# Optimization experiments

Measured on AMD Instinct MI355X. Metric: run time of the kernel, lower is better.

## Reference

```python
import jax, jax.numpy as jnp
import numpy as np

N, E, D, H = 50000, 500000, 128, 128


def setup_inputs() -> dict:
    key = jax.random.key(0)
    ks = jax.random.split(key, 20)
    s = 0.05
    inp = {
        "node_states": jax.random.normal(ks[0], (N, D), jnp.float32),
        "edge_features": jax.random.normal(ks[1], (E, D), jnp.float32),
        "from_idx": jax.random.randint(ks[2], (E,), 0, N, dtype=jnp.int32),
        "to_idx": jax.random.randint(ks[3], (E,), 0, N, dtype=jnp.int32),
        "graph_idx": jax.random.randint(ks[4], (N,), 0, 16, dtype=jnp.int32),
        # message MLP: Linear(3D,H)-ReLU-Linear(H,H)-ReLU-Linear(H,D)
        "mW1": jax.random.normal(ks[5], (3 * D, H), jnp.float32) * s,
        "mb1": jnp.zeros((H,), jnp.float32),
        "mW2": jax.random.normal(ks[6], (H, H), jnp.float32) * s,
        "mb2": jnp.zeros((H,), jnp.float32),
        "mW3": jax.random.normal(ks[7], (H, D), jnp.float32) * s,
        "mb3": jnp.zeros((D,), jnp.float32),
    }
    # three GRU cells; W: input->gates [D,3D], U: hidden->gates [D,3D]; gate order r,z,n (torch)
    for i, g in enumerate(["g0", "g1", "g2"]):
        inp[g + "W"] = jax.random.normal(ks[8 + 2 * i], (D, 3 * D), jnp.float32) * s
        inp[g + "U"] = jax.random.normal(ks[9 + 2 * i], (D, 3 * D), jnp.float32) * s
        inp[g + "b"] = jnp.zeros((3 * D,), jnp.float32)
        inp[g + "c"] = jnp.zeros((3 * D,), jnp.float32)
    return inp


def _mlp(x, W1, b1, W2, b2, W3, b3):
    h = jax.nn.relu(x @ W1 + b1)
    h = jax.nn.relu(h @ W2 + b2)
    return h @ W3 + b3


def _gru(x, h, W, U, b, c):
    gi = x @ W + b  # [N,3D]
    gh = h @ U + c
    ir, iz, inn = jnp.split(gi, 3, axis=1)
    hr, hz, hn = jnp.split(gh, 3, axis=1)
    r = jax.nn.sigmoid(ir + hr)
    z = jax.nn.sigmoid(iz + hz)
    n = jnp.tanh(inn + r * hn)
    return (1.0 - z) * n + z * h


def reference(node_states, edge_features, from_idx, to_idx, graph_idx,
              mW1, mb1, mW2, mb2, mW3, mb3,
              g0W, g0U, g0b, g0c, g1W, g1U, g1b, g1c, g2W, g2U, g2b, g2c):
    n_nodes = node_states.shape[0]

    def prop_once(fi, ti):
        edge_in = jnp.concatenate(
            [node_states[fi], node_states[ti], edge_features], axis=1)  # [E,3D]
        edge_states = _mlp(edge_in, mW1, mb1, mW2, mb2, mW3, mb3)  # [E,D]
        return jax.ops.segment_sum(edge_states, ti, num_segments=n_nodes)

    # forward uses self.message_net for BOTH directions (reverse net unused)
    agg = prop_once(from_idx, to_idx) + prop_once(to_idx, from_idx)  # [N,D]

    h1 = _gru(node_states, agg, g0W, g0U, g0b, g0c)
    h2 = _gru(agg, h1, g1W, g1U, g1b, g1c)
    h3 = _gru(h1, h2, g2W, g2U, g2b, g2c)
    return h3
```

## Files before the change

### kernel.cpp

```cpp
#include <hip/hip_runtime.h>

typedef unsigned short u16;
typedef __attribute__((ext_vector_type(8))) short bf16x8;
typedef __attribute__((ext_vector_type(4))) float f32x4;

__device__ inline u16 f2bf(float f) {
  unsigned int u = __float_as_uint(f);
  u += 0x7fffu + ((u >> 16) & 1u);
  return (u16)(u >> 16);
}
__device__ inline float bf2f(u16 v) {
  return __uint_as_float((unsigned)v << 16);
}

__device__ inline uint4 pack8(float4 a, float4 b) {
  uint4 r;
  r.x = (unsigned)f2bf(a.x) | ((unsigned)f2bf(a.y) << 16);
  r.y = (unsigned)f2bf(a.z) | ((unsigned)f2bf(a.w) << 16);
  r.z = (unsigned)f2bf(b.x) | ((unsigned)f2bf(b.y) << 16);
  r.w = (unsigned)f2bf(b.z) | ((unsigned)f2bf(b.w) << 16);
  return r;
}

struct TransDesc {
  const float* src[9];
  u16* dst[9];
  int R[9];
  int C[9];
  int pre[10];
};

__global__ void transpose_all_kernel(TransDesc td) {
  int t = blockIdx.x * 256 + threadIdx.x;
  if (t >= td.pre[9]) return;
  int seg = 0;
  while (t >= td.pre[seg + 1]) ++seg;
  int local = t - td.pre[seg];
  int C = td.C[seg], R = td.R[seg];
  int r = local / C, c = local - r * C;
  td.dst[seg][(size_t)c * R + r] = f2bf(td.src[seg][local]);
}

__global__ void count_kernel(const int* __restrict__ fi,
                             const int* __restrict__ ti,
                             int* __restrict__ cnt, int E) {
  int e = blockIdx.x * 256 + threadIdx.x;
  if (e < E) {
    atomicAdd(&cnt[ti[e]], 1);
    atomicAdd(&cnt[fi[e]], 1);
  }
}

__global__ void scan1_kernel(const int* __restrict__ cnt,
                             int* __restrict__ partial, int N, int chunk) {
  __shared__ int sdata[256];
  int b = blockIdx.x, t = threadIdx.x;
  int base = b * chunk;
  int sum = 0;
  for (int i = t; i < chunk; i += 256) {
    int idx = base + i;
    if (idx < N) sum += cnt[idx];
  }
  sdata[t] = sum;
  __syncthreads();
  for (int s2 = 128; s2 > 0; s2 >>= 1) {
    if (t < s2) sdata[t] += sdata[t + s2];
    __syncthreads();
  }
  if (t == 0) partial[b] = sdata[0];
}

__global__ void scan2_kernel(int* __restrict__ partial) {
  __shared__ int s[256];
  int t = threadIdx.x;
  int own = partial[t];
  s[t] = own;
  __syncthreads();
  for (int d2 = 1; d2 < 256; d2 <<= 1) {
    int v = (t >= d2) ? s[t - d2] : 0;
    __syncthreads();
    s[t] += v;
    __syncthreads();
  }
  partial[t] = s[t] - own;
}

__global__ void scan3_kernel(const int* __restrict__ cnt,
                             const int* __restrict__ partialEx,
                             int* __restrict__ cursor, int N, int chunk) {
  __shared__ int s[256];
  int b = blockIdx.x, t = threadIdx.x;
  int base = b * chunk;
  int own = (t < chunk && base + t < N) ? cnt[base + t] : 0;
  s[t] = own;
  __syncthreads();
  for (int d2 = 1; d2 < 256; d2 <<= 1) {
    int v = (t >= d2) ? s[t - d2] : 0;
    __syncthreads();
    s[t] += v;
    __syncthreads();
  }
  int ex = s[t] - own + partialEx[b];
  if (t < chunk && base + t < N) cursor[base + t] = ex;
}

__global__ void slot_kernel(const int* __restrict__ fi,
                            const int* __restrict__ ti,
                            int* __restrict__ cursor, int* __restrict__ s_nbr,
                            int* __restrict__ s_eid, int* __restrict__ s_dest,
                            int E) {
  int e = blockIdx.x * 256 + threadIdx.x;
  if (e < E) {
    int f = fi[e], t2 = ti[e];
    int p0 = atomicAdd(&cursor[t2], 1);
    s_nbr[p0] = f;
    s_eid[p0] = e;
    s_dest[p0] = t2;
    int p1 = atomicAdd(&cursor[f], 1);
    s_nbr[p1] = t2;
    s_eid[p1] = e;
    s_dest[p1] = f;
  }
}

__device__ inline void stage_w_rw(u16* sW, const u16* __restrict__ src,
                                  int roww, int colofs, int tid) {
  int n = tid >> 1, half = tid & 1;
  const u16* s = src + (size_t)n * roww + colofs + half * 64;
#pragma unroll
  for (int q = 0; q < 8; ++q) {
    uint4 v = *(const uint4*)(s + q * 8);
    int byte = n * 256 + ((half * 128 + q * 16) ^ ((n & 7) << 4));
    *(uint4*)((char*)sW + byte) = v;
  }
}

__device__ inline void mfma_pass(const u16* A, const u16* W, f32x4 acc[8],
                                 int w, int lane) {
  const int cA = lane & 15;
  const int ko = (lane >> 4) * 8;
  const int arow = 16 * w + cA;
#pragma unroll
  for (int kk = 0; kk < 4; ++kk) {
    int ka = (kk * 32 + ko) * 2;
    int sx = ka ^ ((cA & 7) << 4);
    bf16x8 a = *(const bf16x8*)((const char*)A + arow * 256 + sx);
#pragma unroll
    for (int nt = 0; nt < 8; ++nt) {
      bf16x8 bb = *(const bf16x8*)((const char*)W + (nt * 16 + cA) * 256 + sx);
      acc[nt] = __builtin_amdgcn_mfma_f32_16x16x32_bf16(a, bb, acc[nt], 0, 0, 0);
    }
  }
}

__device__ inline void write_h_lds(u16* sH, const f32x4 acc[8], int w,
                                   int lane) {
#pragma unroll
  for (int nt = 0; nt < 8; ++nt) {
    int col = nt * 16 + (lane & 15);
#pragma unroll
    for (int i = 0; i < 4; ++i) {
      int rr = 16 * w + ((lane >> 4) * 4) + i;
      *(u16*)((char*)sH + rr * 256 + ((col * 2) ^ ((rr & 7) << 4))) =
          f2bf(acc[nt][i]);
    }
  }
}

__global__ __launch_bounds__(256) void node_partial_kernel(
    const float* __restrict__ ns, const u16* __restrict__ Wt1,
    u16* __restrict__ Pa, u16* __restrict__ Pb, int N) {
  __shared__ u16 sA[64 * 128];
  __shared__ u16 sW[128 * 128];
  const int tid = threadIdx.x;
  const int lane = tid & 63;
  const int w = tid >> 6;
  const int r0 = blockIdx.x * 64;
  {
    int row = tid >> 2, seg = tid & 3;
    int rr = r0 + row;
    if (rr >= N) rr = N - 1;
    const float4* sx = (const float4*)(ns + (size_t)rr * 128 + seg * 32);
#pragma unroll
    for (int q = 0; q < 4; ++q) {
      int byte = row * 256 + ((seg * 64 + q * 16) ^ ((row & 7) << 4));
      *(uint4*)((char*)sA + byte) = pack8(sx[q * 2], sx[q * 2 + 1]);
    }
  }
  stage_w_rw(sW, Wt1, 384, 0, tid);
  __syncthreads();
  f32x4 accA[8] = {};
  mfma_pass(sA, sW, accA, w, lane);
  __syncthreads();
  stage_w_rw(sW, Wt1, 384, 128, tid);
  __syncthreads();
  f32x4 accB[8] = {};
  mfma_pass(sA, sW, accB, w, lane);
#pragma unroll
  for (int nt = 0; nt < 8; ++nt) {
    int col = nt * 16 + (lane & 15);
#pragma unroll
    for (int i = 0; i < 4; ++i) {
      int rr = 16 * w + ((lane >> 4) * 4) + i;
      int row = r0 + rr;
      if (row < N) {
        Pa[(size_t)row * 128 + col] = f2bf(accA[nt][i]);
        Pb[(size_t)row * 128 + col] = f2bf(accB[nt][i]);
      }
    }
  }
}

__global__ __launch_bounds__(256) void efgemm_kernel(
    const float* __restrict__ ef, const u16* __restrict__ Wt1,
    const float* __restrict__ b1, u16* __restrict__ EFm, int E) {
  __shared__ u16 sA[64 * 128];
  __shared__ u16 sW[128 * 128];
  const int tid = threadIdx.x;
  const int lane = tid & 63;
  const int w = tid >> 6;
  const int r0 = blockIdx.x * 64;
  {
    int row = tid >> 2, seg = tid & 3;
    int rr = r0 + row;
    if (rr >= E) rr = E - 1;
    const float4* sx = (const float4*)(ef + (size_t)rr * 128 + seg * 32);
#pragma unroll
    for (int q = 0; q < 4; ++q) {
      int byte = row * 256 + ((seg * 64 + q * 16) ^ ((row & 7) << 4));
      *(uint4*)((char*)sA + byte) = pack8(sx[q * 2], sx[q * 2 + 1]);
    }
  }
  stage_w_rw(sW, Wt1, 384, 256, tid);
  __syncthreads();
  f32x4 acc[8] = {};
  mfma_pass(sA, sW, acc, w, lane);
  __syncthreads();
#pragma unroll
  for (int nt = 0; nt < 8; ++nt) {
    int col = nt * 16 + (lane & 15);
    float bv = b1[col];
#pragma unroll
    for (int i = 0; i < 4; ++i) {
      int rr = 16 * w + ((lane >> 4) * 4) + i;
      *(u16*)((char*)sA + rr * 256 + ((col * 2) ^ ((rr & 7) << 4))) =
          f2bf(acc[nt][i] + bv);
    }
  }
  __syncthreads();
#pragma unroll
  for (int it = 0; it < 4; ++it) {
    int task = tid + (it << 8);
    int row = task >> 4, c8 = task & 15;
    int gr = r0 + row;
    if (gr < E) {
      uint4 v = *(const uint4*)((const char*)sA + row * 256 +
                                ((c8 << 4) ^ ((row & 7) << 4)));
      *(uint4*)(EFm + (size_t)gr * 128 + (c8 << 3)) = v;
    }
  }
}

__global__ __launch_bounds__(512, 2) void edge_csr_kernel(
    const u16* __restrict__ EFm, const int* __restrict__ s_nbr,
    const int* __restrict__ s_eid, const int* __restrict__ s_dest,
    const u16* __restrict__ Wt2, const u16* __restrict__ Wt3,
    const u16* __restrict__ Pa, const u16* __restrict__ Pb,
    const float* __restrict__ b2, const float* __restrict__ b3,
    float* __restrict__ aggf, int nslots, int ntiles) {
  __shared__ u16 sH[128 * 128];
  __shared__ int sNbr[128];
  __shared__ int sEid[128];
  __shared__ int sDest[128];
  const int tid = threadIdx.x;
  const int lane = tid & 63;
  const int wv = tid >> 6;
  const int mw = wv >> 1;
  const int nw = wv & 1;
  const int l15 = lane & 15;
  const int lhi = lane >> 4;

  float b2f[4], b3f[4];
#pragma unroll
  for (int nt = 0; nt < 4; ++nt) {
    int col = (nw << 6) + (nt << 4) + l15;
    b2f[nt] = b2[col];
    b3f[nt] = b3[col];
  }
  bf16x8 w2f[4][4], w3f[4][4];
#pragma unroll
  for (int nt = 0; nt < 4; ++nt) {
    int c = (nw << 6) + (nt << 4) + l15;
#pragma unroll
    for (int kk = 0; kk < 4; ++kk) {
      w2f[nt][kk] = *(const bf16x8*)(Wt2 + (size_t)c * 128 + (kk << 5) + (lhi << 3));
      w3f[nt][kk] = *(const bf16x8*)(Wt3 + (size_t)c * 128 + (kk << 5) + (lhi << 3));
    }
  }
  __syncthreads();

  for (int t = blockIdx.x; t < ntiles; t += gridDim.x) {
    const int r0 = t << 7;
    if (tid < 128) {
      int r = r0 + tid;
      int rc = r < nslots ? r : nslots - 1;
      sNbr[tid] = s_nbr[rc];
      sEid[tid] = s_eid[rc];
      sDest[tid] = (r < nslots) ? s_dest[rc] : -1;
    }
    __syncthreads();
#pragma unroll
    for (int it = 0; it < 4; ++it) {
      int row = (tid >> 4) + (it << 5);
      int c8 = tid & 15;
      int nbr = sNbr[row], eid = sEid[row];
      int dst = sDest[row];
      if (dst < 0) dst = 0;
      uint4 efv = *(const uint4*)(EFm + (size_t)eid * 128 + (c8 << 3));
      uint4 pav = *(const uint4*)(Pa + (size_t)nbr * 128 + (c8 << 3));
      uint4 pbv = *(const uint4*)(Pb + (size_t)dst * 128 + (c8 << 3));
      const u16* pe = (const u16*)&efv;
      const u16* pa = (const u16*)&pav;
      const u16* pb = (const u16*)&pbv;
      unsigned o[4];
#pragma unroll
      for (int j = 0; j < 4; ++j) {
        float v0 = fmaxf(bf2f(pe[2 * j]) + bf2f(pa[2 * j]) + bf2f(pb[2 * j]), 0.f);
        float v1 = fmaxf(bf2f(pe[2 * j + 1]) + bf2f(pa[2 * j + 1]) + bf2f(pb[2 * j + 1]), 0.f);
        o[j] = (unsigned)f2bf(v0) | ((unsigned)f2bf(v1) << 16);
      }
      *(uint4*)((char*)sH + row * 256 + ((c8 << 4) ^ ((row & 7) << 4))) = *(uint4*)o;
    }
    __syncthreads();
    bf16x8 hA[2][4];
#pragma unroll
    for (int m = 0; m < 2; ++m) {
      int ra = (mw << 5) + (m << 4) + l15;
#pragma unroll
      for (int kk = 0; kk < 4; ++kk) {
        int sx = ((kk << 6) + (lhi << 4)) ^ ((ra & 7) << 4);
        hA[m][kk] = *(const bf16x8*)((const char*)sH + ra * 256 + sx);
      }
    }
    f32x4 acc2[2][4] = {};
#pragma unroll
    for (int kk = 0; kk < 4; ++kk)
#pragma unroll
      for (int nt = 0; nt < 4; ++nt)
#pragma unroll
        for (int m = 0; m < 2; ++m)
          acc2[m][nt] = __builtin_amdgcn_mfma_f32_16x16x32_bf16(
              hA[m][kk], w2f[nt][kk], acc2[m][nt], 0, 0, 0);
    __syncthreads();
#pragma unroll
    for (int m = 0; m < 2; ++m) {
#pragma unroll
      for (int i = 0; i < 4; ++i) {
        int rl = (mw << 5) + (m << 4) + (lhi << 2) + i;
#pragma unroll
        for (int nt = 0; nt < 4; ++nt) {
          int col = (nw << 6) + (nt << 4) + l15;
          float v = fmaxf(acc2[m][nt][i] + b2f[nt], 0.f);
          *(u16*)((char*)sH + rl * 256 + ((col * 2) ^ ((rl & 7) << 4))) = f2bf(v);
        }
      }
    }
    __syncthreads();
#pragma unroll
    for (int m = 0; m < 2; ++m) {
      int ra = (mw << 5) + (m << 4) + l15;
#pragma unroll
      for (int kk = 0; kk < 4; ++kk) {
        int sx = ((kk << 6) + (lhi << 4)) ^ ((ra & 7) << 4);
        hA[m][kk] = *(const bf16x8*)((const char*)sH + ra * 256 + sx);
      }
    }
    f32x4 acc3[2][4] = {};
#pragma unroll
    for (int kk = 0; kk < 4; ++kk)
#pragma unroll
      for (int nt = 0; nt < 4; ++nt)
#pragma unroll
        for (int m = 0; m < 2; ++m)
          acc3[m][nt] = __builtin_amdgcn_mfma_f32_16x16x32_bf16(
              hA[m][kk], w3f[nt][kk], acc3[m][nt], 0, 0, 0);
    __syncthreads();
#pragma unroll
    for (int m = 0; m < 2; ++m) {
#pragma unroll
      for (int i = 0; i < 4; ++i) {
        int rl = (mw << 5) + (m << 4) + (lhi << 2) + i;
#pragma unroll
        for (int nt = 0; nt < 4; ++nt) {
          int col = (nw << 6) + (nt << 4) + l15;
          *(u16*)((char*)sH + rl * 256 + ((col * 2) ^ ((rl & 7) << 4))) =
              f2bf(acc3[m][nt][i] + b3f[nt]);
        }
      }
    }
    __syncthreads();
    {
      int c = tid & 127, q = tid >> 7;
      float s = 0.f;
      int prev = -1;
      int rbeg = q << 5;
#pragma unroll 4
      for (int rr = rbeg; rr < rbeg + 32; ++rr) {
        int d = sDest[rr];
        if (d != prev) {
          if (prev >= 0) unsafeAtomicAdd(&aggf[(size_t)prev * 128 + c], s);
          prev = d;
          s = 0.f;
        }
        if (d >= 0)
          s += bf2f(*(const u16*)((const char*)sH + rr * 256 +
                                  ((c * 2) ^ ((rr & 7) << 4))));
      }
      if (prev >= 0) unsafeAtomicAdd(&aggf[(size_t)prev * 128 + c], s);
    }
    __syncthreads();
  }
}

__global__ __launch_bounds__(256, 2) void gru3_kernel(
    const float* __restrict__ ns, const float* __restrict__ aggf,
    const u16* __restrict__ g0W, const u16* __restrict__ g0U,
    const u16* __restrict__ g1W, const u16* __restrict__ g1U,
    const u16* __restrict__ g2W, const u16* __restrict__ g2U,
    const float* __restrict__ b0, const float* __restrict__ c0,
    const float* __restrict__ b1, const float* __restrict__ c1,
    const float* __restrict__ b2, const float* __restrict__ c2,
    float* __restrict__ out, int N) {
  __shared__ u16 sX[64 * 128];
  __shared__ u16 sG[64 * 128];
  __shared__ u16 sW[128 * 128];
  const int tid = threadIdx.x;
  const int lane = tid & 63;
  const int w = tid >> 6;
  const int r0 = blockIdx.x * 64;
  {
    int row = tid >> 2, seg = tid & 3;
    int rr = r0 + row;
    if (rr >= N) rr = N - 1;
    const float4* sx = (const float4*)(ns + (size_t)rr * 128 + seg * 32);
    const float4* sh = (const float4*)(aggf + (size_t)rr * 128 + seg * 32);
#pragma unroll
    for (int q = 0; q < 4; ++q) {
      int byte = row * 256 + ((seg * 64 + q * 16) ^ ((row & 7) << 4));
      *(uint4*)((char*)sX + byte) = pack8(sx[q * 2], sx[q * 2 + 1]);
      *(uint4*)((char*)sG + byte) = pack8(sh[q * 2], sh[q * 2 + 1]);
    }
  }

  float hpf[8][4];

#define GPASS(SRC, ABUF, ACC)                       \
  __syncthreads();                                  \
  stage_w_rw(sW, (SRC), 128, 0, tid);               \
  __syncthreads();                                  \
  mfma_pass((ABUF), sW, (ACC), w, lane);

  {
    f32x4 ar[8] = {}, az[8] = {}, ai[8] = {}, ah[8] = {};
    GPASS(g0W + 0 * 16384, sX, ar)
    GPASS(g0U + 0 * 16384, sG, ar)
    GPASS(g0W + 1 * 16384, sX, az)
    GPASS(g0U + 1 * 16384, sG, az)
    GPASS(g0W + 2 * 16384, sX, ai)
    GPASS(g0U + 2 * 16384, sG, ah)
    f32x4 h1[8];
#pragma unroll
    for (int nt = 0; nt < 8; ++nt) {
      int col = nt * 16 + (lane & 15);
      float brc = b0[col] + c0[col];
      float bzc = b0[128 + col] + c0[128 + col];
      float bi = b0[256 + col];
      float bc2 = c0[256 + col];
#pragma unroll
      for (int i = 0; i < 4; ++i) {
        int rloc = 16 * w + ((lane >> 4) * 4) + i;
        int row = r0 + rloc;
        int rowc = row < N ? row : N - 1;
        float hf = aggf[(size_t)rowc * 128 + col];
        float rg = 1.f / (1.f + __expf(-(ar[nt][i] + brc)));
        float zg = 1.f / (1.f + __expf(-(az[nt][i] + bzc)));
        float pre = ai[nt][i] + bi + rg * (ah[nt][i] + bc2);
        float ng = 2.f / (1.f + __expf(-2.f * pre)) - 1.f;
        float hv = (1.f - zg) * ng + zg * hf;
        h1[nt][i] = hv;
        hpf[nt][i] = hv;
      }
    }
    write_h_lds(sX, h1, w, lane);
  }
  {
    f32x4 ar[8] = {}, az[8] = {}, ai[8] = {}, ah[8] = {};
    GPASS(g1W + 0 * 16384, sG, ar)
    GPASS(g1U + 0 * 16384, sX, ar)
    GPASS(g1W + 1 * 16384, sG, az)
    GPASS(g1U + 1 * 16384, sX, az)
    GPASS(g1W + 2 * 16384, sG, ai)
    GPASS(g1U + 2 * 16384, sX, ah)
    f32x4 h2[8];
#pragma unroll
    for (int nt = 0; nt < 8; ++nt) {
      int col = nt * 16 + (lane & 15);
      float brc = b1[col] + c1[col];
      float bzc = b1[128 + col] + c1[128 + col];
      float bi = b1[256 + col];
      float bc2 = c1[256 + col];
#pragma unroll
      for (int i = 0; i < 4; ++i) {
        float rg = 1.f / (1.f + __expf(-(ar[nt][i] + brc)));
        float zg = 1.f / (1.f + __expf(-(az[nt][i] + bzc)));
        float pre = ai[nt][i] + bi + rg * (ah[nt][i] + bc2);
        float ng = 2.f / (1.f + __expf(-2.f * pre)) - 1.f;
        float hv = (1.f - zg) * ng + zg * hpf[nt][i];
        h2[nt][i] = hv;
        hpf[nt][i] = hv;
      }
    }
    write_h_lds(sG, h2, w, lane);
  }
  {
    f32x4 ar[8] = {}, az[8] = {}, ai[8] = {}, ah[8] = {};
    GPASS(g2W + 0 * 16384, sX, ar)
    GPASS(g2U + 0 * 16384, sG, ar)
    GPASS(g2W + 1 * 16384, sX, az)
    GPASS(g2U + 1 * 16384, sG, az)
    GPASS(g2W + 2 * 16384, sX, ai)
    GPASS(g2U + 2 * 16384, sG, ah)
#pragma unroll
    for (int nt = 0; nt < 8; ++nt) {
      int col = nt * 16 + (lane & 15);
      float brc = b2[col] + c2[col];
      float bzc = b2[128 + col] + c2[128 + col];
      float bi = b2[256 + col];
      float bc2 = c2[256 + col];
#pragma unroll
      for (int i = 0; i < 4; ++i) {
        int rloc = 16 * w + ((lane >> 4) * 4) + i;
        int row = r0 + rloc;
        if (row < N) {
          float rg = 1.f / (1.f + __expf(-(ar[nt][i] + brc)));
          float zg = 1.f / (1.f + __expf(-(az[nt][i] + bzc)));
          float pre = ai[nt][i] + bi + rg * (ah[nt][i] + bc2);
          float ng = 2.f / (1.f + __expf(-2.f * pre)) - 1.f;
          out[(size_t)row * 128 + col] = (1.f - zg) * ng + zg * hpf[nt][i];
        }
      }
    }
  }
#undef GPASS
}

extern "C" void kernel_launch(void* const* d_in, const int* in_sizes, int n_in,
                              void* d_out, int out_size, void* d_ws,
                              size_t ws_size, hipStream_t stream) {
  const float* ns = (const float*)d_in[0];
  const float* ef = (const float*)d_in[1];
  const int* from_idx = (const int*)d_in[2];
  const int* to_idx = (const int*)d_in[3];
  const float* mW1 = (const float*)d_in[5];
  const float* mb1 = (const float*)d_in[6];
  const float* mW2 = (const float*)d_in[7];
  const float* mb2 = (const float*)d_in[8];
  const float* mW3 = (const float*)d_in[9];
  const float* mb3 = (const float*)d_in[10];
  const float* gW[3] = {(const float*)d_in[11], (const float*)d_in[15], (const float*)d_in[19]};
  const float* gU[3] = {(const float*)d_in[12], (const float*)d_in[16], (const float*)d_in[20]};
  const float* gb[3] = {(const float*)d_in[13], (const float*)d_in[17], (const float*)d_in[21]};
  const float* gc[3] = {(const float*)d_in[14], (const float*)d_in[18], (const float*)d_in[22]};

  const int N = in_sizes[0] / 128;
  const int E = in_sizes[1] / 128;
  const int nslots = 2 * E;

  char* base = (char*)d_ws;
  size_t cur = 0;
  auto alloc = [&](size_t bytes) {
    size_t p = cur;
    cur = (cur + bytes + 255) & ~(size_t)255;
    return (void*)(base + p);
  };
  float* aggf = (float*)alloc((size_t)N * 128 * 4);
  u16* Pa = (u16*)alloc((size_t)N * 128 * 2);
  u16* Pb = (u16*)alloc((size_t)N * 128 * 2);
  u16* Wt1 = (u16*)alloc(384 * 128 * 2);
  u16* Wt2 = (u16*)alloc(128 * 128 * 2);
  u16* Wt3 = (u16*)alloc(128 * 128 * 2);
  u16 *gWt[3], *gUt[3];
  for (int i = 0; i < 3; ++i) {
    gWt[i] = (u16*)alloc(384 * 128 * 2);
    gUt[i] = (u16*)alloc(384 * 128 * 2);
  }
  int* cnt = (int*)alloc((size_t)N * 4);
  int* cursor = (int*)alloc((size_t)N * 4);
  int* partial = (int*)alloc(256 * 4);
  int* s_nbr = (int*)alloc((size_t)nslots * 4);
  int* s_eid = (int*)alloc((size_t)nslots * 4);
  int* s_dest = (int*)alloc((size_t)nslots * 4);
  u16* EFm = (u16*)alloc((size_t)E * 128 * 2);
  (void)ws_size;

  {
    TransDesc td;
    const float* srcs[9] = {mW1, mW2, mW3, gW[0], gU[0], gW[1], gU[1], gW[2], gU[2]};
    u16* dsts[9] = {Wt1, Wt2, Wt3, gWt[0], gUt[0], gWt[1], gUt[1], gWt[2], gUt[2]};
    int Rs[9] = {384, 128, 128, 128, 128, 128, 128, 128, 128};
    int Cs[9] = {128, 128, 128, 384, 384, 384, 384, 384, 384};
    int acc = 0;
    for (int i = 0; i < 9; ++i) {
      td.src[i] = srcs[i];
      td.dst[i] = dsts[i];
      td.R[i] = Rs[i];
      td.C[i] = Cs[i];
      td.pre[i] = acc;
      acc += Rs[i] * Cs[i];
    }
    td.pre[9] = acc;
    transpose_all_kernel<<<(acc + 255) / 256, 256, 0, stream>>>(td);
  }

  node_partial_kernel<<<(N + 63) / 64, 256, 0, stream>>>(ns, Wt1, Pa, Pb, N);

  hipMemsetAsync(cnt, 0, (size_t)N * 4, stream);
  count_kernel<<<(E + 255) / 256, 256, 0, stream>>>(from_idx, to_idx, cnt, E);
  int chunk = (N + 255) / 256;
  scan1_kernel<<<256, 256, 0, stream>>>(cnt, partial, N, chunk);
  scan2_kernel<<<1, 256, 0, stream>>>(partial);
  scan3_kernel<<<256, 256, 0, stream>>>(cnt, partial, cursor, N, chunk);
  slot_kernel<<<(E + 255) / 256, 256, 0, stream>>>(from_idx, to_idx, cursor,
                                                   s_nbr, s_eid, s_dest, E);

  efgemm_kernel<<<(E + 63) / 64, 256, 0, stream>>>(ef, Wt1, mb1, EFm, E);

  hipMemsetAsync(aggf, 0, (size_t)N * 128 * 4, stream);
  int ntiles = (nslots + 127) / 128;
  int egrid = ntiles < 512 ? ntiles : 512;
  edge_csr_kernel<<<egrid, 512, 0, stream>>>(EFm, s_nbr, s_eid, s_dest, Wt2,
                                             Wt3, Pa, Pb, mb2, mb3, aggf,
                                             nslots, ntiles);

  int gblocks = (N + 63) / 64;
  gru3_kernel<<<gblocks, 256, 0, stream>>>(
      ns, aggf, gWt[0], gUt[0], gWt[1], gUt[1], gWt[2], gUt[2], gb[0], gc[0],
      gb[1], gc[1], gb[2], gc[2], (float*)d_out, N);
}
```

Baseline: 648.9 us.

## Prefetch next edge tile's gathers into LDS asynchronously and widen efgemm tiles

The edge MLP kernel now loads the next tile's slot metadata into registers. It then issues that tile's EFm, Pa and Pb row gathers straight into three new LDS buffers with global_load_lds, so the gather latency overlaps with the current tile's two MFMA layers and the atomic scatter. The extra 96 KB of LDS leaves room for only one 512-thread block per CU, so the persistent grid is cut to 256 blocks. Separately, the edge-feature GEMM now processes 128 rows per 512-thread block, with a matching weight-staging helper. Risks are lower occupancy, and the reliance on correct vmcnt waiting before the prefetched LDS data is read.

Measured after the change: 640.2 us. No clear change (-1.3%).

```diff
diff --git a/kernel.cpp b/kernel.cpp
--- a/kernel.cpp
+++ b/kernel.cpp
@@ -20,6 +20,12 @@
   r.z = (unsigned)f2bf(b.x) | ((unsigned)f2bf(b.y) << 16);
   r.w = (unsigned)f2bf(b.z) | ((unsigned)f2bf(b.w) << 16);
   return r;
+}
+
+__device__ inline void gload_lds16(const void* g, void* l) {
+  __builtin_amdgcn_global_load_lds(
+      (const __attribute__((address_space(1))) unsigned int*)g,
+      (__attribute__((address_space(3))) unsigned int*)l, 16, 0, 0);
 }
 
 struct TransDesc {
@@ -135,6 +141,18 @@
   }
 }
 
+__device__ inline void stage_w_512(u16* sW, const u16* __restrict__ src,
+                                   int roww, int colofs, int tid) {
+  int n = tid >> 2, quarter = tid & 3;
+  const u16* s = src + (size_t)n * roww + colofs + quarter * 32;
+#pragma unroll
+  for (int q = 0; q < 4; ++q) {
+    uint4 v = *(const uint4*)(s + q * 8);
+    int byte = n * 256 + ((quarter * 64 + q * 16) ^ ((n & 7) << 4));
+    *(uint4*)((char*)sW + byte) = v;
+  }
+}
+
 __device__ inline void mfma_pass(const u16* A, const u16* W, f32x4 acc[8],
                                  int w, int lane) {
   const int cA = lane & 15;
@@ -211,15 +229,15 @@
   }
 }
 
-__global__ __launch_bounds__(256) void efgemm_kernel(
+__global__ __launch_bounds__(512) void efgemm_kernel(
     const float* __restrict__ ef, const u16* __restrict__ Wt1,
     const float* __restrict__ b1, u16* __restrict__ EFm, int E) {
-  __shared__ u16 sA[64 * 128];
+  __shared__ u16 sA[128 * 128];
   __shared__ u16 sW[128 * 128];
   const int tid = threadIdx.x;
   const int lane = tid & 63;
   const int w = tid >> 6;
-  const int r0 = blockIdx.x * 64;
+  const int r0 = blockIdx.x * 128;
   {
     int row = tid >> 2, seg = tid & 3;
     int rr = r0 + row;
@@ -231,7 +249,7 @@
       *(uint4*)((char*)sA + byte) = pack8(sx[q * 2], sx[q * 2 + 1]);
     }
   }
-  stage_w_rw(sW, Wt1, 384, 256, tid);
+  stage_w_512(sW, Wt1, 384, 256, tid);
   __syncthreads();
   f32x4 acc[8] = {};
   mfma_pass(sA, sW, acc, w, lane);
@@ -250,7 +268,7 @@
   __syncthreads();
 #pragma unroll
   for (int it = 0; it < 4; ++it) {
-    int task = tid + (it << 8);
+    int task = tid + (it << 9);
     int row = task >> 4, c8 = task & 15;
     int gr = r0 + row;
     if (gr < E) {
@@ -269,8 +287,9 @@
     const float* __restrict__ b2, const float* __restrict__ b3,
     float* __restrict__ aggf, int nslots, int ntiles) {
   __shared__ u16 sH[128 * 128];
-  __shared__ int sNbr[128];
-  __shared__ int sEid[128];
+  __shared__ u16 sPreEF[128 * 128];
+  __shared__ u16 sPrePA[128 * 128];
+  __shared__ u16 sPrePB[128 * 128];
   __shared__ int sDest[128];
   const int tid = threadIdx.x;
   const int lane = tid & 63;
@@ -279,6 +298,8 @@
   const int nw = wv & 1;
   const int l15 = lane & 15;
   const int lhi = lane >> 4;
+  const int c8 = tid & 15;
+  const int wbase = (tid >> 6) << 10;
 
   float b2f[4], b3f[4];
 #pragma unroll
@@ -297,28 +318,54 @@
       w3f[nt][kk] = *(const bf16x8*)(Wt3 + (size_t)c * 128 + (kk << 5) + (lhi << 3));
     }
   }
-  __syncthreads();
-
-  for (int t = blockIdx.x; t < ntiles; t += gridDim.x) {
-    const int r0 = t << 7;
-    if (tid < 128) {
-      int r = r0 + tid;
+
+  int nbr4[4], eid4[4], dst4[4];
+  auto load_meta = [&](int tt) {
+#pragma unroll
+    for (int it = 0; it < 4; ++it) {
+      int r = (tt << 7) + (tid >> 4) + (it << 5);
       int rc = r < nslots ? r : nslots - 1;
-      sNbr[tid] = s_nbr[rc];
-      sEid[tid] = s_eid[rc];
-      sDest[tid] = (r < nslots) ? s_dest[rc] : -1;
-    }
-    __syncthreads();
+      nbr4[it] = s_nbr[rc];
+      eid4[it] = s_eid[rc];
+      dst4[it] = (r < nslots) ? s_dest[rc] : -1;
+    }
+  };
+  auto issue_gathers = [&]() {
+#pragma unroll
+    for (int it = 0; it < 4; ++it) {
+      int dd = dst4[it] < 0 ? 0 : dst4[it];
+      int off = wbase + (it << 13);
+      gload_lds16(EFm + (size_t)eid4[it] * 128 + (c8 << 3), (char*)sPreEF + off);
+      gload_lds16(Pa + (size_t)nbr4[it] * 128 + (c8 << 3), (char*)sPrePA + off);
+      gload_lds16(Pb + (size_t)dd * 128 + (c8 << 3), (char*)sPrePB + off);
+    }
+  };
+  auto write_dest = [&]() {
+    if ((tid & 15) == 0) {
+#pragma unroll
+      for (int it = 0; it < 4; ++it) sDest[(tid >> 4) + (it << 5)] = dst4[it];
+    }
+  };
+
+  int t = blockIdx.x;
+  if (t < ntiles) {
+    load_meta(t);
+    issue_gathers();
+    write_dest();
+  }
+  __syncthreads();
+
+  for (; t < ntiles; t += gridDim.x) {
+    const int tn = t + gridDim.x;
+    const bool has_next = tn < ntiles;
+    if (has_next) load_meta(tn);
 #pragma unroll
     for (int it = 0; it < 4; ++it) {
       int row = (tid >> 4) + (it << 5);
-      int c8 = tid & 15;
-      int nbr = sNbr[row], eid = sEid[row];
-      int dst = sDest[row];
-      if (dst < 0) dst = 0;
-      uint4 efv = *(const uint4*)(EFm + (size_t)eid * 128 + (c8 << 3));
-      uint4 pav = *(const uint4*)(Pa + (size_t)nbr * 128 + (c8 << 3));
-      uint4 pbv = *(const uint4*)(Pb + (size_t)dst * 128 + (c8 << 3));
+      int boff = row * 256 + (c8 << 4);
+      uint4 efv = *(const uint4*)((const char*)sPreEF + boff);
+      uint4 pav = *(const uint4*)((const char*)sPrePA + boff);
+      uint4 pbv = *(const uint4*)((const char*)sPrePB + boff);
       const u16* pe = (const u16*)&efv;
       const u16* pa = (const u16*)&pav;
       const u16* pb = (const u16*)&pbv;
@@ -332,6 +379,7 @@
       *(uint4*)((char*)sH + row * 256 + ((c8 << 4) ^ ((row & 7) << 4))) = *(uint4*)o;
     }
     __syncthreads();
+    if (has_next) issue_gathers();
     bf16x8 hA[2][4];
 #pragma unroll
     for (int m = 0; m < 2; ++m) {
@@ -342,15 +390,15 @@
         hA[m][kk] = *(const bf16x8*)((const char*)sH + ra * 256 + sx);
       }
     }
-    f32x4 acc2[2][4] = {};
+    f32x4 acc[2][4] = {};
 #pragma unroll
     for (int kk = 0; kk < 4; ++kk)
 #pragma unroll
       for (int nt = 0; nt < 4; ++nt)
 #pragma unroll
         for (int m = 0; m < 2; ++m)
-          acc2[m][nt] = __builtin_amdgcn_mfma_f32_16x16x32_bf16(
-              hA[m][kk], w2f[nt][kk], acc2[m][nt], 0, 0, 0);
+          acc[m][nt] = __builtin_amdgcn_mfma_f32_16x16x32_bf16(
+              hA[m][kk], w2f[nt][kk], acc[m][nt], 0, 0, 0);
     __syncthreads();
 #pragma unroll
     for (int m = 0; m < 2; ++m) {
@@ -360,8 +408,9 @@
 #pragma unroll
         for (int nt = 0; nt < 4; ++nt) {
           int col = (nw << 6) + (nt << 4) + l15;
-          float v = fmaxf(acc2[m][nt][i] + b2f[nt], 0.f);
+          float v = fmaxf(acc[m][nt][i] + b2f[nt], 0.f);
           *(u16*)((char*)sH + rl * 256 + ((col * 2) ^ ((rl & 7) << 4))) = f2bf(v);
+          acc[m][nt][i] = 0.f;
         }
       }
     }
@@ -375,15 +424,14 @@
         hA[m][kk] = *(const bf16x8*)((const char*)sH + ra * 256 + sx);
       }
     }
-    f32x4 acc3[2][4] = {};
 #pragma unroll
     for (int kk = 0; kk < 4; ++kk)
 #pragma unroll
       for (int nt = 0; nt < 4; ++nt)
 #pragma unroll
         for (int m = 0; m < 2; ++m)
-          acc3[m][nt] = __builtin_amdgcn_mfma_f32_16x16x32_bf16(
-              hA[m][kk], w3f[nt][kk], acc3[m][nt], 0, 0, 0);
+          acc[m][nt] = __builtin_amdgcn_mfma_f32_16x16x32_bf16(
+              hA[m][kk], w3f[nt][kk], acc[m][nt], 0, 0, 0);
     __syncthreads();
 #pragma unroll
     for (int m = 0; m < 2; ++m) {
@@ -394,7 +442,7 @@
         for (int nt = 0; nt < 4; ++nt) {
           int col = (nw << 6) + (nt << 4) + l15;
           *(u16*)((char*)sH + rl * 256 + ((col * 2) ^ ((rl & 7) << 4))) =
-              f2bf(acc3[m][nt][i] + b3f[nt]);
+              f2bf(acc[m][nt][i] + b3f[nt]);
         }
       }
     }
@@ -419,6 +467,7 @@
       if (prev >= 0) unsafeAtomicAdd(&aggf[(size_t)prev * 128 + c], s);
     }
     __syncthreads();
+    if (has_next) write_dest();
   }
 }
 
@@ -633,11 +682,11 @@
   slot_kernel<<<(E + 255) / 256, 256, 0, stream>>>(from_idx, to_idx, cursor,
                                                    s_nbr, s_eid, s_dest, E);
 
-  efgemm_kernel<<<(E + 63) / 64, 256, 0, stream>>>(ef, Wt1, mb1, EFm, E);
+  efgemm_kernel<<<(E + 127) / 128, 512, 0, stream>>>(ef, Wt1, mb1, EFm, E);
 
   hipMemsetAsync(aggf, 0, (size_t)N * 128 * 4, stream);
   int ntiles = (nslots + 127) / 128;
-  int egrid = ntiles < 512 ? ntiles : 512;
+  int egrid = ntiles < 256 ? ntiles : 256;
   edge_csr_kernel<<<egrid, 512, 0, stream>>>(EFm, s_nbr, s_eid, s_dest, Wt2,
                                              Wt3, Pa, Pb, mb2, mb3, aggf,
                                              nslots, ntiles);
```
